# Performance work log

Hardware: AMD Instinct MI355X
Metric: run time of the kernel (lower is better)

The kernel has to match this reference:

```python
import jax, jax.numpy as jnp
import numpy as np
from jax import lax

B, N, C = 4, 1024, 384
H, G, K = 6, 2, 10
GD = C // G   # group dim = 192
HD = C // H   # head dim = 64
SCALE = HD ** -0.5
LN_EPS = 1e-5


def _sqdist(a, b):
    # a: [..., M, 3], b: [..., N, 3] -> squared euclid dist [..., M, N]
    return (jnp.sum(a * a, -1)[..., :, None]
            - 2.0 * jnp.einsum('...mc,...nc->...mn', a, b)
            + jnp.sum(b * b, -1)[..., None, :])


def _layernorm(x, g, b):
    mu = jnp.mean(x, -1, keepdims=True)
    var = jnp.mean(jnp.square(x - mu), -1, keepdims=True)
    return (x - mu) * lax.rsqrt(var + LN_EPS) * g + b


def _forward(q, q_pos, Wq, Wk, Wv, Wvoff, W1, b1, ln_g, ln_b, W2, Wproj, bproj):
    # self-attention path: v = q, v_pos = q_pos
    bidx = jnp.arange(B)[:, None, None]
    # KNN over positions: idx [B, N, K]
    d = _sqdist(q_pos, q_pos)
    _, idx = lax.top_k(-d, K)
    qp = q @ Wq                       # [B, N, C]
    v_off = q @ Wvoff                 # [B, N, C]
    local_v = v_off[bidx, idx]        # [B, N, K, C]
    # split channels into groups: 'b n k (g c) -> b g n k c'
    off_local_v = local_v.reshape(B, N, K, G, GD).transpose(0, 3, 1, 2, 4)
    group_q = qp.reshape(B, N, G, GD).transpose(0, 2, 1, 3)      # [B, G, N, GD]
    shift_feat = jnp.concatenate(
        [off_local_v, jnp.broadcast_to(group_q[:, :, :, None, :], (B, G, N, K, GD))], -1)
    h = _layernorm(shift_feat @ W1 + b1, ln_g, ln_b)
    h = jax.nn.gelu(h, approximate=False)
    offset = jnp.tanh(h @ W2)                                    # [B, G, N, K, 3]
    local_v_pos = q_pos[bidx, idx]                               # [B, N, K, 3]
    shift_pos = (local_v_pos[:, None] + offset).reshape(B, G, N * K, 3)
    # three_nn: 3 nearest v_pos points for each shifted point (squared dists, as in CUDA kernel)
    v_pos_g = jnp.broadcast_to(q_pos[:, None], (B, G, N, 3))
    d2 = _sqdist(shift_pos, v_pos_g)                             # [B, G, N*K, N]
    neg_d3, idx3 = lax.top_k(-d2, 3)
    dist3 = -neg_d3                                              # ascending
    rec = 1.0 / (dist3 + 1e-8)
    w = rec / jnp.sum(rec, -1, keepdims=True)                    # [B, G, N*K, 3]
    # three_interpolate on grouped v features
    v_g = q.reshape(B, N, G, GD).transpose(0, 2, 1, 3)           # [B, G, N, GD]
    gathered = v_g[jnp.arange(B)[:, None, None, None],
                   jnp.arange(G)[None, :, None, None], idx3]      # [B, G, N*K, 3, GD]
    interp = jnp.sum(w[..., None] * gathered, 3)                 # [B, G, N*K, GD]
    # '(b g) (n k) c -> b n k (g c)'
    interp = interp.reshape(B, G, N, K, GD).transpose(0, 2, 3, 1, 4).reshape(B, N, K, C)
    # local cross attention: 1 query vs K keys per token per head
    kk = (interp @ Wk).reshape(B, N, K, H, HD)
    vv = (interp @ Wv).reshape(B, N, K, H, HD)
    qh = qp.reshape(B, N, H, HD)
    attn = jnp.einsum('bnhd,bnkhd->bnhk', qh, kk) * SCALE
    attn = jax.nn.softmax(attn, -1)
    out = jnp.einsum('bnhk,bnkhd->bnhd', attn, vv).reshape(B, N, C)
    return out @ Wproj + bproj


def setup_inputs() -> dict:
    key = jax.random.key(0)
    ks = jax.random.split(key, 12)
    s = 0.02
    return {
        'q': jax.random.normal(ks[0], (B, N, C), jnp.float32),
        'q_pos': jax.random.normal(ks[1], (B, N, 3), jnp.float32),
        'Wq': s * jax.random.normal(ks[2], (C, C), jnp.float32),
        'Wk': s * jax.random.normal(ks[3], (C, C), jnp.float32),
        'Wv': s * jax.random.normal(ks[4], (C, C), jnp.float32),
        'Wvoff': s * jax.random.normal(ks[5], (C, C), jnp.float32),
        'W1': s * jax.random.normal(ks[6], (2 * GD, C), jnp.float32),
        'b1': jnp.zeros((C,), jnp.float32),
        'ln_g': jnp.ones((C,), jnp.float32),
        'ln_b': jnp.zeros((C,), jnp.float32),
        'W2': s * jax.random.normal(ks[7], (C, 3), jnp.float32),
        'Wproj': s * jax.random.normal(ks[8], (C, C), jnp.float32),
        'bproj': jnp.zeros((C,), jnp.float32),
    }


def reference(q, q_pos, Wq, Wk, Wv, Wvoff, W1, b1, ln_g, ln_b, W2, Wproj, bproj):
    return _forward(q, q_pos, Wq, Wk, Wv, Wvoff, W1, b1, ln_g, ln_b, W2, Wproj, bproj)
```

## Files before the change

### kernel.cpp

```cpp
#include <hip/hip_runtime.h>
#include <math.h>

constexpr int B_ = 4;
constexpr int N_ = 1024;
constexpr int C_ = 384;
constexpr int G_ = 2;
constexpr int K_ = 10;
constexpr int GD_ = 192;
constexpr int NK_ = N_ * K_;
constexpr int M2_ = B_ * G_ * N_ * K_;
constexpr float SCALE_ = 0.125f;
constexpr float MARGIN_ = 4e-4f;

constexpr int L1_PREPM_ = G_ * C_;
constexpr int L1_GRID_ = L1_PREPM_ + 11;
constexpr int L2_KNN_ = 683;
constexpr int L2_GRID_ = L2_KNN_ + 512;

__device__ __forceinline__ bool lless(double da, int ia, double db, int ib) {
  return (da < db) || (da == db && ia < ib);
}
__device__ __forceinline__ void lmin2(double& rd, int& ri, double ad, int ai,
                                      double bd, int bi) {
  bool t = lless(bd, bi, ad, ai);
  rd = t ? bd : ad; ri = t ? bi : ai;
}
__device__ __forceinline__ void lmax2(double& rd, int& ri, double ad, int ai,
                                      double bd, int bi) {
  bool t = lless(ad, ai, bd, bi);
  rd = t ? bd : ad; ri = t ? bi : ai;
}
__device__ __forceinline__ void pmin2(float& rd, int& ri, float ad, int ai,
                                      float bd, int bi) {
  bool t = bd < ad;
  rd = t ? bd : ad; ri = t ? bi : ai;
}
__device__ __forceinline__ void pmax2(float& rd, int& ri, float ad, int ai,
                                      float bd, int bi) {
  bool t = ad < bd;
  rd = t ? bd : ad; ri = t ? bi : ai;
}
__device__ __forceinline__ float ftanh(float p) {
  float pc = fminf(fmaxf(p, -15.f), 15.f);
  float e = __expf(2.f * pc);
  return (e - 1.f) * __builtin_amdgcn_rcpf(e + 1.f);
}

__global__ __launch_bounds__(384) void k_L1(const float* __restrict__ Wvoff,
                                            const float* __restrict__ Wq,
                                            const float* __restrict__ W1,
                                            const float* __restrict__ Wk,
                                            const float* __restrict__ q_pos,
                                            float* __restrict__ M1f,
                                            float* __restrict__ M2f,
                                            float* __restrict__ WkT,
                                            double* __restrict__ s64,
                                            float4* __restrict__ pos4,
                                            int* __restrict__ cnt) {
  if (blockIdx.x < L1_PREPM_) {
    int g = blockIdx.x / C_;
    int k = blockIdx.x % C_;
    int c = threadIdx.x;
    if (g == 0) WkT[c * C_ + k] = Wk[k * C_ + c];
    const float* wv = Wvoff + k * C_ + g * GD_;
    const float* wq = Wq + k * C_ + g * GD_;
    double a1 = 0.0, a2 = 0.0;
    for (int d = 0; d < GD_; d++) {
      a1 += (double)wv[d] * (double)W1[d * C_ + c];
      a2 += (double)wq[d] * (double)W1[(GD_ + d) * C_ + c];
    }
    M1f[(g * C_ + k) * C_ + c] = (float)a1;
    M2f[(g * C_ + k) * C_ + c] = (float)a2;
  } else {
    int i = (blockIdx.x - L1_PREPM_) * 384 + threadIdx.x;
    if (i == 0) cnt[0] = 0;
    if (i >= B_ * N_) return;
    float x = q_pos[3 * i], y = q_pos[3 * i + 1], z = q_pos[3 * i + 2];
    double v = (double)x * x + (double)y * y + (double)z * z;
    s64[i] = v;
    pos4[i] = make_float4(x, y, z, (float)v);
  }
}

__global__ __launch_bounds__(384) void k_L2a(const float* __restrict__ q_pos,
                                             const double* __restrict__ s,
                                             int* __restrict__ idx10,
                                             const float* __restrict__ q,
                                             const float* __restrict__ Wq,
                                             float* __restrict__ qp) {
  if (blockIdx.x < L2_KNN_) {
    int wid = blockIdx.x * 6 + (threadIdx.x >> 6);
    int lane = threadIdx.x & 63;
    if (wid >= B_ * N_) return;
    int b = wid / N_;
    double px = q_pos[3 * wid], py = q_pos[3 * wid + 1], pz = q_pos[3 * wid + 2];
    double sm = s[wid];
    const float* bp = q_pos + b * N_ * 3;
    const double* bs = s + b * N_;
    double d[K_]; int ix[K_];
    #pragma unroll
    for (int j = 0; j < K_; j++) { d[j] = INFINITY; ix[j] = 0x7fffffff; }
    for (int n0 = 0; n0 < N_; n0 += 64) {
      int n = n0 + lane;
      double dot = px * (double)bp[3 * n] + py * (double)bp[3 * n + 1] +
                   pz * (double)bp[3 * n + 2];
      double v = (sm - 2.0 * dot) + bs[n];
      bool c[K_];
      #pragma unroll
      for (int j = 0; j < K_; j++) c[j] = lless(v, n, d[j], ix[j]);
      #pragma unroll
      for (int j = K_ - 1; j >= 1; j--) {
        d[j]  = c[j] ? (c[j - 1] ? d[j - 1] : v) : d[j];
        ix[j] = c[j] ? (c[j - 1] ? ix[j - 1] : n) : ix[j];
      }
      d[0]  = c[0] ? v : d[0];
      ix[0] = c[0] ? n : ix[0];
    }
    #pragma unroll
    for (int off = 1; off < 64; off <<= 1) {
      double bd[K_]; int bi[K_];
      #pragma unroll
      for (int j = 0; j < K_; j++) {
        bd[j] = __shfl_xor(d[j], off);
        bi[j] = __shfl_xor(ix[j], off);
      }
      double md[K_]; int mi[K_];
      #pragma unroll
      for (int r = 0; r < K_; r++) {
        double m; int mj;
        lmin2(m, mj, d[r], ix[r], bd[r], bi[r]);
        #pragma unroll
        for (int j = 1; j <= r; j++) {
          double t; int ti;
          lmax2(t, ti, d[j - 1], ix[j - 1], bd[r - j], bi[r - j]);
          lmin2(m, mj, m, mj, t, ti);
        }
        md[r] = m; mi[r] = mj;
      }
      #pragma unroll
      for (int j = 0; j < K_; j++) { d[j] = md[j]; ix[j] = mi[j]; }
    }
    if (lane == 0) {
      #pragma unroll
      for (int j = 0; j < K_; j++) idx10[wid * K_ + j] = ix[j];
    }
  } else {
    int c = threadIdx.x;
    int r0 = (blockIdx.x - L2_KNN_) * 8;
    float acc[8];
    #pragma unroll
    for (int r = 0; r < 8; r++) acc[r] = 0.f;
    #pragma unroll 4
    for (int j = 0; j < C_; j++) {
      float w = Wq[j * C_ + c];
      #pragma unroll
      for (int r = 0; r < 8; r++) acc[r] = fmaf(q[(r0 + r) * C_ + j], w, acc[r]);
    }
    #pragma unroll
    for (int r = 0; r < 8; r++) qp[(r0 + r) * C_ + c] = acc[r];
  }
}

__global__ __launch_bounds__(384) void k_Y32(const float* __restrict__ q,
                                             const float* __restrict__ M1f,
                                             const float* __restrict__ M2f,
                                             float* __restrict__ Y1f,
                                             float* __restrict__ Y2f) {
  int c = threadIdx.x;
  int g = blockIdx.y;
  int r0 = blockIdx.x * 8;
  float a1[8], a2[8];
  #pragma unroll
  for (int r = 0; r < 8; r++) { a1[r] = 0.f; a2[r] = 0.f; }
  const float* m1 = M1f + (size_t)(g * C_) * C_ + c;
  const float* m2 = M2f + (size_t)(g * C_) * C_ + c;
  for (int k = 0; k < C_; k++) {
    float v1 = m1[(size_t)k * C_];
    float v2 = m2[(size_t)k * C_];
    #pragma unroll
    for (int r = 0; r < 8; r++) {
      float av = q[(r0 + r) * C_ + k];
      a1[r] = fmaf(av, v1, a1[r]);
      a2[r] = fmaf(av, v2, a2[r]);
    }
  }
  #pragma unroll
  for (int r = 0; r < 8; r++) {
    Y1f[((size_t)(r0 + r) * G_ + g) * C_ + c] = a1[r];
    Y2f[((size_t)(r0 + r) * G_ + g) * C_ + c] = a2[r];
  }
}

__global__ __launch_bounds__(384) void k_mlptop4(const float* __restrict__ Y1f,
                                                 const float* __restrict__ Y2f,
                                                 const int* __restrict__ idx10,
                                                 const float* __restrict__ q_pos,
                                                 const float* __restrict__ b1,
                                                 const float* __restrict__ ln_g,
                                                 const float* __restrict__ ln_b,
                                                 const float* __restrict__ W2,
                                                 const float4* __restrict__ pos4,
                                                 const float* __restrict__ q,
                                                 float* __restrict__ interp,
                                                 int* __restrict__ flags,
                                                 int* __restrict__ cnt) {
  int w_ = threadIdx.x >> 6, l = threadIdx.x & 63;
  int row = blockIdx.x * 6 + w_;
  if (row >= M2_) return;
  int k = row % K_; int t = row / K_;
  int n = t % N_; t /= N_;
  int g = t % G_; int b = t / G_;
  int j = idx10[(b * N_ + n) * K_ + k];
  const float* y1 = Y1f + ((size_t)(b * N_ + j) * G_ + g) * C_;
  const float* y2 = Y2f + ((size_t)(b * N_ + n) * G_ + g) * C_;
  float x[6];
  #pragma unroll
  for (int jj = 0; jj < 6; jj++) {
    int col = l + 64 * jj;
    x[jj] = y1[col] + y2[col] + b1[col];
  }
  float sum = ((((x[0] + x[1]) + x[2]) + x[3]) + x[4]) + x[5];
  #pragma unroll
  for (int off = 1; off < 64; off <<= 1) sum += __shfl_xor(sum, off);
  float mu = sum * (1.0f / 384.0f);
  float sq = 0.f;
  #pragma unroll
  for (int jj = 0; jj < 6; jj++) { float dd = x[jj] - mu; sq = fmaf(dd, dd, sq); }
  #pragma unroll
  for (int off = 1; off < 64; off <<= 1) sq += __shfl_xor(sq, off);
  float var = sq * (1.0f / 384.0f);
  float rstd = 1.0f / sqrtf(var + 1e-5f);
  float ge[6];
  #pragma unroll
  for (int jj = 0; jj < 6; jj++) {
    int col = l + 64 * jj;
    float nv = (x[jj] - mu) * rstd * ln_g[col] + ln_b[col];
    ge[jj] = 0.5f * nv * (1.0f + erff(nv * 0.70710678118654752f));
  }
  float o3[3];
  #pragma unroll
  for (int o = 0; o < 3; o++) {
    float p = 0.f;
    #pragma unroll
    for (int jj = 0; jj < 6; jj++) {
      int col = l + 64 * jj;
      p = fmaf(ge[jj], W2[col * 3 + o], p);
    }
    #pragma unroll
    for (int off = 1; off < 64; off <<= 1) p += __shfl_xor(p, off);
    o3[o] = ftanh(p);
  }
  int gi = b * N_ + j;
  float px = q_pos[gi * 3 + 0] + o3[0];
  float py = q_pos[gi * 3 + 1] + o3[1];
  float pz = q_pos[gi * 3 + 2] + o3[2];
  float sp = fmaf(px, px, fmaf(py, py, pz * pz));
  float nx = -2.0f * px, ny = -2.0f * py, nz = -2.0f * pz;
  const float4* p4 = pos4 + b * N_;
  float d0 = INFINITY, d1 = INFINITY, d2 = INFINITY, r4 = INFINITY;
  int i0 = 0x7fffffff, i1 = 0x7fffffff, i2 = 0x7fffffff;
  for (int n0 = 0; n0 < N_; n0 += 64) {
    int nn = n0 + l;
    float4 pv = p4[nn];
    float v = fmaf(nx, pv.x, fmaf(ny, pv.y, fmaf(nz, pv.z, sp + pv.w)));
    bool c0 = v < d0, c1 = v < d1, c2 = v < d2;
    float disp = c2 ? d2 : v;
    r4 = fminf(r4, disp);
    d2 = c2 ? (c1 ? d1 : v) : d2;
    i2 = c2 ? (c1 ? i1 : nn) : i2;
    d1 = c1 ? (c0 ? d0 : v) : d1;
    i1 = c1 ? (c0 ? i0 : nn) : i1;
    d0 = c0 ? v : d0;
    i0 = c0 ? nn : i0;
  }
  #pragma unroll
  for (int off = 1; off < 64; off <<= 1) {
    float e0 = __shfl_xor(d0, off), e1 = __shfl_xor(d1, off), e2 = __shfl_xor(d2, off);
    float er = __shfl_xor(r4, off);
    int j0 = __shfl_xor(i0, off), j1 = __shfl_xor(i1, off), j2 = __shfl_xor(i2, off);
    float va = fmaxf(d0, e2), vb = fmaxf(d1, e1), vc = fmaxf(d2, e0);
    float r4n = fminf(fminf(r4, er), fminf(fminf(va, vb), vc));
    float m0d, t1d, u1d, m1d, t2a, t2b, u2d, w2d, m2d;
    int m0i, t1i, u1i, m1i, t2ai, t2bi, u2i, w2i, m2i;
    pmin2(m0d, m0i, d0, i0, e0, j0);
    pmax2(t1d, t1i, d0, i0, e0, j0);
    pmin2(u1d, u1i, d1, i1, e1, j1);
    pmin2(m1d, m1i, u1d, u1i, t1d, t1i);
    pmax2(t2a, t2ai, d1, i1, e0, j0);
    pmax2(t2b, t2bi, d0, i0, e1, j1);
    pmin2(u2d, u2i, d2, i2, e2, j2);
    pmin2(w2d, w2i, t2a, t2ai, t2b, t2bi);
    pmin2(m2d, m2i, u2d, u2i, w2d, w2i);
    d0 = m0d; i0 = m0i; d1 = m1d; i1 = m1i; d2 = m2d; i2 = m2i; r4 = r4n;
  }
  if (r4 - d2 < MARGIN_) {
    if (l == 0) {
      int pos = atomicAdd(cnt, 1);
      flags[pos] = row;
    }
    return;
  }
  float r0 = 1.0f / (d0 + 1e-8f);
  float r1 = 1.0f / (d1 + 1e-8f);
  float r2 = 1.0f / (d2 + 1e-8f);
  float rs = (r0 + r1) + r2;
  float w0 = r0 / rs, w1 = r1 / rs, w2 = r2 / rs;
  const float* qb = q + (size_t)b * N_ * C_ + g * GD_;
  const float* p0 = qb + (size_t)i0 * C_;
  const float* p1 = qb + (size_t)i1 * C_;
  const float* p2 = qb + (size_t)i2 * C_;
  float* op = interp + (((size_t)(b * N_ + n) * K_ + k) * C_) + g * GD_;
  #pragma unroll
  for (int cc0 = 0; cc0 < GD_; cc0 += 64) {
    int cc = cc0 + l;
    op[cc] = (w0 * p0[cc] + w1 * p1[cc]) + w2 * p2[cc];
  }
}

__global__ __launch_bounds__(256) void k_fix(const int* __restrict__ cnt,
                                             const int* __restrict__ flags,
                                             const float* __restrict__ q,
                                             const float* __restrict__ Wvoff,
                                             const float* __restrict__ Wq,
                                             const float* __restrict__ W1,
                                             const int* __restrict__ idx10,
                                             const float* __restrict__ q_pos,
                                             const double* __restrict__ s64,
                                             const float* __restrict__ b1,
                                             const float* __restrict__ ln_g,
                                             const float* __restrict__ ln_b,
                                             const float* __restrict__ W2,
                                             float* __restrict__ interp) {
  __shared__ double vbuf[4][2][GD_];
  int w_ = threadIdx.x >> 6;
  int gwid = blockIdx.x * 4 + w_;
  int lane = threadIdx.x & 63;
  int nwaves = gridDim.x * 4;
  int total = cnt[0];
  for (int i = gwid; i < total; i += nwaves) {
    int wid = __builtin_amdgcn_readfirstlane(flags[i]);
    int m = wid % NK_; int t = wid / NK_;
    int g = t % G_; int b = t / G_;
    int n_ = m / K_, k_ = m % K_;
    int j = __builtin_amdgcn_readfirstlane(idx10[(b * N_ + n_) * K_ + k_]);
    const float* qj = q + (size_t)(b * N_ + j) * C_;
    const float* qn = q + (size_t)(b * N_ + n_) * C_;
    const float* wvo = Wvoff + g * GD_;
    const float* wqg = Wq + g * GD_;
    double a0 = 0.0, a1 = 0.0, a2 = 0.0, b0 = 0.0, b1a = 0.0, b2 = 0.0;
    for (int tt = 0; tt < C_; tt++) {
      double qjt = (double)qj[tt];
      double qnt = (double)qn[tt];
      const float* r1 = wvo + (size_t)tt * C_;
      const float* r2 = wqg + (size_t)tt * C_;
      a0 += qjt * (double)r1[lane];
      a1 += qjt * (double)r1[lane + 64];
      a2 += qjt * (double)r1[lane + 128];
      b0 += qnt * (double)r2[lane];
      b1a += qnt * (double)r2[lane + 64];
      b2 += qnt * (double)r2[lane + 128];
    }
    vbuf[w_][0][lane] = a0; vbuf[w_][0][lane + 64] = a1; vbuf[w_][0][lane + 128] = a2;
    vbuf[w_][1][lane] = b0; vbuf[w_][1][lane + 64] = b1a; vbuf[w_][1][lane + 128] = b2;
    double x[6];
    #pragma unroll
    for (int jj = 0; jj < 6; jj++) x[jj] = 0.0;
    for (int d = 0; d < GD_; d++) {
      double v1d = vbuf[w_][0][d];
      double v2d = vbuf[w_][1][d];
      const float* w1t = W1 + (size_t)d * C_;
      const float* w1b = W1 + (size_t)(GD_ + d) * C_;
      #pragma unroll
      for (int jj = 0; jj < 6; jj++) {
        int col = lane + 64 * jj;
        x[jj] += v1d * (double)w1t[col] + v2d * (double)w1b[col];
      }
    }
    #pragma unroll
    for (int jj = 0; jj < 6; jj++) x[jj] += (double)b1[lane + 64 * jj];
    double sum = ((((x[0] + x[1]) + x[2]) + x[3]) + x[4]) + x[5];
    #pragma unroll
    for (int off = 1; off < 64; off <<= 1) sum += __shfl_xor(sum, off);
    double mu = sum / 384.0;
    double sq = 0.0;
    #pragma unroll
    for (int jj = 0; jj < 6; jj++) { double dd = x[jj] - mu; sq += dd * dd; }
    #pragma unroll
    for (int off = 1; off < 64; off <<= 1) sq += __shfl_xor(sq, off);
    double var = sq / 384.0;
    double rstd = 1.0 / sqrt(var + 1e-5);
    double ge[6];
    #pragma unroll
    for (int jj = 0; jj < 6; jj++) {
      int col = lane + 64 * jj;
      double nv = (x[jj] - mu) * rstd * (double)ln_g[col] + (double)ln_b[col];
      ge[jj] = 0.5 * nv * (1.0 + erf(nv * 0.70710678118654752440));
    }
    double o3[3];
    #pragma unroll
    for (int o = 0; o < 3; o++) {
      double p = 0.0;
      #pragma unroll
      for (int jj = 0; jj < 6; jj++) {
        int col = lane + 64 * jj;
        p += ge[jj] * (double)W2[col * 3 + o];
      }
      #pragma unroll
      for (int off = 1; off < 64; off <<= 1) p += __shfl_xor(p, off);
      o3[o] = tanh(p);
    }
    int gi = b * N_ + j;
    double px = (double)q_pos[gi * 3 + 0] + o3[0];
    double py = (double)q_pos[gi * 3 + 1] + o3[1];
    double pz = (double)q_pos[gi * 3 + 2] + o3[2];
    double sp = px * px + py * py + pz * pz;
    const float* bp = q_pos + b * N_ * 3;
    const double* bs = s64 + b * N_;
    double d0 = INFINITY, d1 = INFINITY, d2 = INFINITY;
    int i0 = 0x7fffffff, i1 = 0x7fffffff, i2 = 0x7fffffff;
    for (int n = lane; n < N_; n += 64) {
      double dot = px * (double)bp[3 * n] + py * (double)bp[3 * n + 1] +
                   pz * (double)bp[3 * n + 2];
      double dd = (sp - 2.0 * dot) + bs[n];
      bool c0 = lless(dd, n, d0, i0);
      bool c1 = lless(dd, n, d1, i1);
      bool c2 = lless(dd, n, d2, i2);
      double nd2 = c2 ? (c1 ? d1 : dd) : d2; int ni2 = c2 ? (c1 ? i1 : n) : i2;
      double nd1 = c1 ? (c0 ? d0 : dd) : d1; int ni1 = c1 ? (c0 ? i0 : n) : i1;
      double nd0 = c0 ? dd : d0;             int ni0 = c0 ? n : i0;
      d0 = nd0; d1 = nd1; d2 = nd2; i0 = ni0; i1 = ni1; i2 = ni2;
    }
    #pragma unroll
    for (int off = 1; off < 64; off <<= 1) {
      double e0 = __shfl_xor(d0, off), e1 = __shfl_xor(d1, off), e2 = __shfl_xor(d2, off);
      int j0 = __shfl_xor(i0, off), j1 = __shfl_xor(i1, off), j2 = __shfl_xor(i2, off);
      double mnd, mxd, p1d, q1d, q2d, q3d, q4d, t1d, t2d;
      int mni, mxi, p1i, q1i, q2i, q3i, q4i, t1i, t2i;
      lmin2(mnd, mni, d0, i0, e0, j0);
      lmax2(mxd, mxi, d0, i0, e0, j0);
      lmin2(p1d, p1i, d1, i1, e1, j1);
      lmin2(t1d, t1i, p1d, p1i, mxd, mxi);
      lmax2(q1d, q1i, d1, i1, e0, j0);
      lmax2(q2d, q2i, d0, i0, e1, j1);
      lmin2(q3d, q3i, q1d, q1i, q2d, q2i);
      lmin2(q4d, q4i, d2, i2, e2, j2);
      lmin2(t2d, t2i, q3d, q3i, q4d, q4i);
      d0 = mnd; i0 = mni; d1 = t1d; i1 = t1i; d2 = t2d; i2 = t2i;
    }
    double r0 = 1.0 / (d0 + 1e-8);
    double r1 = 1.0 / (d1 + 1e-8);
    double r2 = 1.0 / (d2 + 1e-8);
    double rs = (r0 + r1) + r2;
    float w0 = (float)(r0 / rs), w1 = (float)(r1 / rs), w2 = (float)(r2 / rs);
    const float* qb = q + (size_t)b * N_ * C_ + g * GD_;
    const float* p0 = qb + (size_t)i0 * C_;
    const float* p1 = qb + (size_t)i1 * C_;
    const float* p2 = qb + (size_t)i2 * C_;
    float* op = interp + (((size_t)(b * N_ + n_) * K_ + k_) * C_) + g * GD_;
    #pragma unroll
    for (int cc0 = 0; cc0 < GD_; cc0 += 64) {
      int cc = cc0 + lane;
      op[cc] = (w0 * p0[cc] + w1 * p1[cc]) + w2 * p2[cc];
    }
  }
}

__global__ __launch_bounds__(384) void k_U(const float* __restrict__ qp,
                                           const float* __restrict__ WkT,
                                           float* __restrict__ U) {
  int c = threadIdx.x;
  int r0 = blockIdx.x * 8;
  for (int h = 0; h < 6; h++) {
    float acc[8];
    #pragma unroll
    for (int r = 0; r < 8; r++) acc[r] = 0.f;
    #pragma unroll 4
    for (int dd = 0; dd < 64; dd++) {
      float w = WkT[(h * 64 + dd) * C_ + c];
      #pragma unroll
      for (int r = 0; r < 8; r++)
        acc[r] = fmaf(qp[(r0 + r) * C_ + h * 64 + dd], w, acc[r]);
    }
    #pragma unroll
    for (int r = 0; r < 8; r++) U[((size_t)(r0 + r) * 6 + h) * C_ + c] = acc[r];
  }
}

__global__ __launch_bounds__(384) void k_attn2(const float* __restrict__ interp,
                                               float* __restrict__ Umix) {
  int bn = blockIdx.x * 6 + (threadIdx.x >> 6);
  int lane = threadIdx.x & 63;
  if (bn >= B_ * N_) return;
  float ipv[K_][6];
  const float* ip0 = interp + (size_t)bn * K_ * C_;
  #pragma unroll
  for (int k = 0; k < K_; k++) {
    #pragma unroll
    for (int j = 0; j < 6; j++) ipv[k][j] = ip0[k * C_ + lane + 64 * j];
  }
  float* ubase = Umix + (size_t)bn * 6 * C_;
  for (int h = 0; h < 6; h++) {
    float u[6];
    #pragma unroll
    for (int j = 0; j < 6; j++) u[j] = ubase[h * C_ + lane + 64 * j];
    float logit[K_];
    #pragma unroll
    for (int k = 0; k < K_; k++) {
      float p = 0.f;
      #pragma unroll
      for (int j = 0; j < 6; j++) p = fmaf(ipv[k][j], u[j], p);
      #pragma unroll
      for (int off = 1; off < 64; off <<= 1) p += __shfl_xor(p, off);
      logit[k] = p * SCALE_;
    }
    float mx = logit[0];
    #pragma unroll
    for (int k = 1; k < K_; k++) mx = fmaxf(mx, logit[k]);
    float e[K_], se = 0.f;
    #pragma unroll
    for (int k = 0; k < K_; k++) { e[k] = __expf(logit[k] - mx); se += e[k]; }
    float inv = 1.0f / se;
    #pragma unroll
    for (int k = 0; k < K_; k++) e[k] *= inv;
    #pragma unroll
    for (int j = 0; j < 6; j++) {
      float mv = 0.f;
      #pragma unroll
      for (int k = 0; k < K_; k++) mv = fmaf(e[k], ipv[k][j], mv);
      ubase[h * C_ + lane + 64 * j] = mv;
    }
  }
}

__global__ __launch_bounds__(384) void k_outproj(const float* __restrict__ mix,
                                                 const float* __restrict__ Wv,
                                                 const float* __restrict__ Wproj,
                                                 const float* __restrict__ bproj,
                                                 float* __restrict__ out) {
  __shared__ float ao[8][C_];
  int c = threadIdx.x;
  int h = __builtin_amdgcn_readfirstlane(threadIdx.x) >> 6;
  int r0 = blockIdx.x * 8;
  float acc[8];
  #pragma unroll
  for (int r = 0; r < 8; r++) acc[r] = 0.f;
  #pragma unroll 4
  for (int ci = 0; ci < C_; ci++) {
    float w = Wv[ci * C_ + c];
    #pragma unroll
    for (int r = 0; r < 8; r++)
      acc[r] = fmaf(mix[((size_t)(r0 + r) * 6 + h) * C_ + ci], w, acc[r]);
  }
  #pragma unroll
  for (int r = 0; r < 8; r++) ao[r][c] = acc[r];
  __syncthreads();
  float a2[8];
  #pragma unroll
  for (int r = 0; r < 8; r++) a2[r] = 0.f;
  #pragma unroll 4
  for (int ci = 0; ci < C_; ci++) {
    float w = Wproj[ci * C_ + c];
    #pragma unroll
    for (int r = 0; r < 8; r++) a2[r] = fmaf(ao[r][ci], w, a2[r]);
  }
  float bv = bproj[c];
  #pragma unroll
  for (int r = 0; r < 8; r++) out[(size_t)(r0 + r) * C_ + c] = a2[r] + bv;
}

extern "C" void kernel_launch(void* const* d_in, const int* in_sizes, int n_in,
                              void* d_out, int out_size, void* d_ws, size_t ws_size,
                              hipStream_t stream) {
  const float* q     = (const float*)d_in[0];
  const float* q_pos = (const float*)d_in[1];
  const float* Wq    = (const float*)d_in[2];
  const float* Wk    = (const float*)d_in[3];
  const float* Wv    = (const float*)d_in[4];
  const float* Wvoff = (const float*)d_in[5];
  const float* W1    = (const float*)d_in[6];
  const float* b1    = (const float*)d_in[7];
  const float* ln_g  = (const float*)d_in[8];
  const float* ln_b  = (const float*)d_in[9];
  const float* W2    = (const float*)d_in[10];
  const float* Wproj = (const float*)d_in[11];
  const float* bproj = (const float*)d_in[12];
  float* out = (float*)d_out;

  char* ws = (char*)d_ws;
  char* U0 = ws; ws += 38 * 1024 * 1024;
  float*  Y1f    = (float*)(U0);
  float*  Y2f    = (float*)(U0 + 12582912);
  float*  M1f    = (float*)(U0 + 25165824);
  float*  M2f    = (float*)(U0 + 26345472);
  float*  Umix   = (float*)U0;
  double* s64    = (double*)ws; ws += (size_t)B_ * N_ * 8;
  float*  qp32   = (float*)ws;  ws += (size_t)B_ * N_ * C_ * 4;
  float*  interp = (float*)ws;  ws += (size_t)B_ * N_ * K_ * C_ * 4;
  float*  WkT    = (float*)ws;  ws += (size_t)C_ * C_ * 4;
  int*    idx10  = (int*)ws;    ws += (size_t)B_ * N_ * K_ * 4;
  int*    flags  = (int*)ws;    ws += (size_t)M2_ * 4;
  float4* pos4   = (float4*)ws; ws += (size_t)B_ * N_ * 16;
  int*    cnt    = (int*)ws;    ws += 256;

  k_L1<<<L1_GRID_, 384, 0, stream>>>(Wvoff, Wq, W1, Wk, q_pos, M1f, M2f, WkT,
                                     s64, pos4, cnt);
  k_L2a<<<L2_GRID_, 384, 0, stream>>>(q_pos, s64, idx10, q, Wq, qp32);
  k_Y32<<<dim3(B_ * N_ / 8, G_), 384, 0, stream>>>(q, M1f, M2f, Y1f, Y2f);
  k_mlptop4<<<(M2_ + 5) / 6, 384, 0, stream>>>(Y1f, Y2f, idx10, q_pos, b1, ln_g,
                                               ln_b, W2, pos4, q, interp, flags,
                                               cnt);
  k_fix<<<512, 256, 0, stream>>>(cnt, flags, q, Wvoff, Wq, W1, idx10, q_pos, s64,
                                 b1, ln_g, ln_b, W2, interp);
  k_U<<<B_ * N_ / 8, 384, 0, stream>>>(qp32, WkT, Umix);
  k_attn2<<<(B_ * N_ + 5) / 6, 384, 0, stream>>>(interp, Umix);
  k_outproj<<<B_ * N_ / 8, 384, 0, stream>>>(Umix, Wv, Wproj, bproj, out);
}
```

Before: 665.9 us.

## Split fused KNN/Wq kernel, enlarge Y32 row tile, resize mlptop4 blocks

Splits the fused KNN and q@Wq kernel into two launches: a KNN kernel using 256-thread blocks (4 queries per block) and a standalone GEMM. The Y32 GEMM now computes 16 rows per block instead of 8, reusing each loaded M1f/M2f value across more rows at the cost of more registers. The MLP/top-4 kernel moves to 256-thread blocks with 4 rows each and drops the bounds check, since the row count divides evenly. The extra launch adds overhead, and the larger accumulator arrays may reduce occupancy.

```diff
diff --git a/kernel.cpp b/kernel.cpp
--- a/kernel.cpp
+++ b/kernel.cpp
@@ -14,8 +14,6 @@
 
 constexpr int L1_PREPM_ = G_ * C_;
 constexpr int L1_GRID_ = L1_PREPM_ + 11;
-constexpr int L2_KNN_ = 683;
-constexpr int L2_GRID_ = L2_KNN_ + 512;
 
 __device__ __forceinline__ bool lless(double da, int ia, double db, int ib) {
   return (da < db) || (da == db && ia < ib);
@@ -82,83 +80,82 @@
   }
 }
 
-__global__ __launch_bounds__(384) void k_L2a(const float* __restrict__ q_pos,
-                                             const double* __restrict__ s,
-                                             int* __restrict__ idx10,
-                                             const float* __restrict__ q,
-                                             const float* __restrict__ Wq,
-                                             float* __restrict__ qp) {
-  if (blockIdx.x < L2_KNN_) {
-    int wid = blockIdx.x * 6 + (threadIdx.x >> 6);
-    int lane = threadIdx.x & 63;
-    if (wid >= B_ * N_) return;
-    int b = wid / N_;
-    double px = q_pos[3 * wid], py = q_pos[3 * wid + 1], pz = q_pos[3 * wid + 2];
-    double sm = s[wid];
-    const float* bp = q_pos + b * N_ * 3;
-    const double* bs = s + b * N_;
-    double d[K_]; int ix[K_];
-    #pragma unroll
-    for (int j = 0; j < K_; j++) { d[j] = INFINITY; ix[j] = 0x7fffffff; }
-    for (int n0 = 0; n0 < N_; n0 += 64) {
-      int n = n0 + lane;
-      double dot = px * (double)bp[3 * n] + py * (double)bp[3 * n + 1] +
-                   pz * (double)bp[3 * n + 2];
-      double v = (sm - 2.0 * dot) + bs[n];
-      bool c[K_];
-      #pragma unroll
-      for (int j = 0; j < K_; j++) c[j] = lless(v, n, d[j], ix[j]);
-      #pragma unroll
-      for (int j = K_ - 1; j >= 1; j--) {
-        d[j]  = c[j] ? (c[j - 1] ? d[j - 1] : v) : d[j];
-        ix[j] = c[j] ? (c[j - 1] ? ix[j - 1] : n) : ix[j];
+__global__ __launch_bounds__(256) void k_knn10_w(const float* __restrict__ q_pos,
+                                                 const double* __restrict__ s,
+                                                 int* __restrict__ idx10) {
+  int wid = (blockIdx.x * blockDim.x + threadIdx.x) >> 6;
+  int lane = threadIdx.x & 63;
+  if (wid >= B_ * N_) return;
+  int b = wid / N_;
+  double px = q_pos[3 * wid], py = q_pos[3 * wid + 1], pz = q_pos[3 * wid + 2];
+  double sm = s[wid];
+  const float* bp = q_pos + b * N_ * 3;
+  const double* bs = s + b * N_;
+  double d[K_]; int ix[K_];
+  #pragma unroll
+  for (int j = 0; j < K_; j++) { d[j] = INFINITY; ix[j] = 0x7fffffff; }
+  for (int n0 = 0; n0 < N_; n0 += 64) {
+    int n = n0 + lane;
+    double dot = px * (double)bp[3 * n] + py * (double)bp[3 * n + 1] +
+                 pz * (double)bp[3 * n + 2];
+    double v = (sm - 2.0 * dot) + bs[n];
+    bool c[K_];
+    #pragma unroll
+    for (int j = 0; j < K_; j++) c[j] = lless(v, n, d[j], ix[j]);
+    #pragma unroll
+    for (int j = K_ - 1; j >= 1; j--) {
+      d[j]  = c[j] ? (c[j - 1] ? d[j - 1] : v) : d[j];
+      ix[j] = c[j] ? (c[j - 1] ? ix[j - 1] : n) : ix[j];
+    }
+    d[0]  = c[0] ? v : d[0];
+    ix[0] = c[0] ? n : ix[0];
+  }
+  #pragma unroll
+  for (int off = 1; off < 64; off <<= 1) {
+    double bd[K_]; int bi[K_];
+    #pragma unroll
+    for (int j = 0; j < K_; j++) {
+      bd[j] = __shfl_xor(d[j], off);
+      bi[j] = __shfl_xor(ix[j], off);
+    }
+    double md[K_]; int mi[K_];
+    #pragma unroll
+    for (int r = 0; r < K_; r++) {
+      double m; int mj;
+      lmin2(m, mj, d[r], ix[r], bd[r], bi[r]);
+      #pragma unroll
+      for (int j = 1; j <= r; j++) {
+        double t; int ti;
+        lmax2(t, ti, d[j - 1], ix[j - 1], bd[r - j], bi[r - j]);
+        lmin2(m, mj, m, mj, t, ti);
       }
-      d[0]  = c[0] ? v : d[0];
-      ix[0] = c[0] ? n : ix[0];
-    }
-    #pragma unroll
-    for (int off = 1; off < 64; off <<= 1) {
-      double bd[K_]; int bi[K_];
-      #pragma unroll
-      for (int j = 0; j < K_; j++) {
-        bd[j] = __shfl_xor(d[j], off);
-        bi[j] = __shfl_xor(ix[j], off);
-      }
-      double md[K_]; int mi[K_];
-      #pragma unroll
-      for (int r = 0; r < K_; r++) {
-        double m; int mj;
-        lmin2(m, mj, d[r], ix[r], bd[r], bi[r]);
-        #pragma unroll
-        for (int j = 1; j <= r; j++) {
-          double t; int ti;
-          lmax2(t, ti, d[j - 1], ix[j - 1], bd[r - j], bi[r - j]);
-          lmin2(m, mj, m, mj, t, ti);
-        }
-        md[r] = m; mi[r] = mj;
-      }
-      #pragma unroll
-      for (int j = 0; j < K_; j++) { d[j] = md[j]; ix[j] = mi[j]; }
-    }
-    if (lane == 0) {
-      #pragma unroll
-      for (int j = 0; j < K_; j++) idx10[wid * K_ + j] = ix[j];
-    }
-  } else {
-    int c = threadIdx.x;
-    int r0 = (blockIdx.x - L2_KNN_) * 8;
-    float acc[8];
-    #pragma unroll
-    for (int r = 0; r < 8; r++) acc[r] = 0.f;
-    #pragma unroll 4
-    for (int j = 0; j < C_; j++) {
-      float w = Wq[j * C_ + c];
-      #pragma unroll
-      for (int r = 0; r < 8; r++) acc[r] = fmaf(q[(r0 + r) * C_ + j], w, acc[r]);
-    }
-    #pragma unroll
-    for (int r = 0; r < 8; r++) qp[(r0 + r) * C_ + c] = acc[r];
-  }
+      md[r] = m; mi[r] = mj;
+    }
+    #pragma unroll
+    for (int j = 0; j < K_; j++) { d[j] = md[j]; ix[j] = mi[j]; }
+  }
+  if (lane == 0) {
+    #pragma unroll
+    for (int j = 0; j < K_; j++) idx10[wid * K_ + j] = ix[j];
+  }
+}
+
+__global__ __launch_bounds__(384) void k_gemmSA(const float* __restrict__ A,
+                                                const float* __restrict__ W,
+                                                float* __restrict__ out) {
+  int c = threadIdx.x;
+  int r0 = blockIdx.x * 8;
+  float acc[8];
+  #pragma unroll
+  for (int r = 0; r < 8; r++) acc[r] = 0.f;
+  #pragma unroll 4
+  for (int j = 0; j < C_; j++) {
+    float w = W[j * C_ + c];
+    #pragma unroll
+    for (int r = 0; r < 8; r++) acc[r] = fmaf(A[(r0 + r) * C_ + j], w, acc[r]);
+  }
+  #pragma unroll
+  for (int r = 0; r < 8; r++) out[(r0 + r) * C_ + c] = acc[r];
 }
 
 __global__ __launch_bounds__(384) void k_Y32(const float* __restrict__ q,
@@ -166,32 +163,33 @@
                                              const float* __restrict__ M2f,
                                              float* __restrict__ Y1f,
                                              float* __restrict__ Y2f) {
+  constexpr int TM = 16;
   int c = threadIdx.x;
   int g = blockIdx.y;
-  int r0 = blockIdx.x * 8;
-  float a1[8], a2[8];
-  #pragma unroll
-  for (int r = 0; r < 8; r++) { a1[r] = 0.f; a2[r] = 0.f; }
+  int r0 = blockIdx.x * TM;
+  float a1[TM], a2[TM];
+  #pragma unroll
+  for (int r = 0; r < TM; r++) { a1[r] = 0.f; a2[r] = 0.f; }
   const float* m1 = M1f + (size_t)(g * C_) * C_ + c;
   const float* m2 = M2f + (size_t)(g * C_) * C_ + c;
   for (int k = 0; k < C_; k++) {
     float v1 = m1[(size_t)k * C_];
     float v2 = m2[(size_t)k * C_];
     #pragma unroll
-    for (int r = 0; r < 8; r++) {
+    for (int r = 0; r < TM; r++) {
       float av = q[(r0 + r) * C_ + k];
       a1[r] = fmaf(av, v1, a1[r]);
       a2[r] = fmaf(av, v2, a2[r]);
     }
   }
   #pragma unroll
-  for (int r = 0; r < 8; r++) {
+  for (int r = 0; r < TM; r++) {
     Y1f[((size_t)(r0 + r) * G_ + g) * C_ + c] = a1[r];
     Y2f[((size_t)(r0 + r) * G_ + g) * C_ + c] = a2[r];
   }
 }
 
-__global__ __launch_bounds__(384) void k_mlptop4(const float* __restrict__ Y1f,
+__global__ __launch_bounds__(256) void k_mlptop4(const float* __restrict__ Y1f,
                                                  const float* __restrict__ Y2f,
                                                  const int* __restrict__ idx10,
                                                  const float* __restrict__ q_pos,
@@ -205,8 +203,7 @@
                                                  int* __restrict__ flags,
                                                  int* __restrict__ cnt) {
   int w_ = threadIdx.x >> 6, l = threadIdx.x & 63;
-  int row = blockIdx.x * 6 + w_;
-  if (row >= M2_) return;
+  int row = blockIdx.x * 4 + w_;
   int k = row % K_; int t = row / K_;
   int n = t % N_; t /= N_;
   int g = t % G_; int b = t / G_;
@@ -604,11 +601,11 @@
 
   k_L1<<<L1_GRID_, 384, 0, stream>>>(Wvoff, Wq, W1, Wk, q_pos, M1f, M2f, WkT,
                                      s64, pos4, cnt);
-  k_L2a<<<L2_GRID_, 384, 0, stream>>>(q_pos, s64, idx10, q, Wq, qp32);
-  k_Y32<<<dim3(B_ * N_ / 8, G_), 384, 0, stream>>>(q, M1f, M2f, Y1f, Y2f);
-  k_mlptop4<<<(M2_ + 5) / 6, 384, 0, stream>>>(Y1f, Y2f, idx10, q_pos, b1, ln_g,
-                                               ln_b, W2, pos4, q, interp, flags,
-                                               cnt);
+  k_knn10_w<<<B_ * N_ / 4, 256, 0, stream>>>(q_pos, s64, idx10);
+  k_gemmSA<<<B_ * N_ / 8, 384, 0, stream>>>(q, Wq, qp32);
+  k_Y32<<<dim3(B_ * N_ / 16, G_), 384, 0, stream>>>(q, M1f, M2f, Y1f, Y2f);
+  k_mlptop4<<<M2_ / 4, 256, 0, stream>>>(Y1f, Y2f, idx10, q_pos, b1, ln_g, ln_b,
+                                         W2, pos4, q, interp, flags, cnt);
   k_fix<<<512, 256, 0, stream>>>(cnt, flags, q, Wvoff, Wq, W1, idx10, q_pos, s64,
                                  b1, ln_g, ln_b, W2, interp);
   k_U<<<B_ * N_ / 8, 384, 0, stream>>>(qp32, WkT, Umix);
```

New measurement: 676.9 us. About the same (+1.6%).
